# Performance work log

Measured on AMD Instinct MI355X. Metric: run time of the kernel, lower is better.

Reference implementation:

```python
import jax, jax.numpy as jnp
import numpy as np


def _grad(x, axis):
    """torch.gradient with unit spacing: central diff interior, one-sided edges."""
    def sl(a, b):
        idx = [slice(None)] * x.ndim
        idx[axis] = slice(a, b)
        return x[tuple(idx)]
    left = sl(1, 2) - sl(0, 1)                 # (x[1]-x[0])
    mid = (sl(2, None) - sl(0, -2)) * 0.5      # (x[i+1]-x[i-1])/2
    right = sl(-1, None) - sl(-2, -1)          # (x[-1]-x[-2])
    return jnp.concatenate([left, mid, right], axis=axis)


def _mse0(e):
    return jnp.mean(e * e)  # MSE against zeros


def _phy_loss(V_all, P_all, F_all, Re):
    Vy = V_all[:, :, :, :, 0, :]
    Vx = V_all[:, :, :, :, 1, :]
    Vz = V_all[:, :, :, :, 2, :]
    Fy = F_all[:, :, :, :, 0, :]
    Fx = F_all[:, :, :, :, 1, :]
    Fz = F_all[:, :, :, :, 2, :]
    # first derivatives (dims: 1=y, 2=x, 3=z, 4=t)
    dVydt, dVydy, dVydx, dVydz = _grad(Vy, 4), _grad(Vy, 1), _grad(Vy, 2), _grad(Vy, 3)
    dVxdt, dVxdy, dVxdx, dVxdz = _grad(Vx, 4), _grad(Vx, 1), _grad(Vx, 2), _grad(Vx, 3)
    dVzdt, dVzdy, dVzdx, dVzdz = _grad(Vz, 4), _grad(Vz, 1), _grad(Vz, 2), _grad(Vz, 3)
    dPdx, dPdy, dPdz = _grad(P_all, 2), _grad(P_all, 1), _grad(P_all, 3)
    # second derivatives
    lapVx = _grad(dVxdx, 2) + _grad(dVxdy, 1) + _grad(dVxdz, 3)
    lapVy = _grad(dVydx, 2) + _grad(dVydy, 1) + _grad(dVydz, 3)
    lapVz = _grad(dVzdx, 2) + _grad(dVzdy, 1) + _grad(dVzdz, 3)
    e1 = dVydt + (Vx * dVydx + Vy * dVydy + Vz * dVydz + dPdy) - Re * lapVy + Fy
    e2 = dVxdt + (Vx * dVxdx + Vy * dVxdy + Vz * dVxdz + dPdx) - Re * lapVx + Fx
    e3 = dVzdt + (Vx * dVzdx + Vy * dVzdy + Vz * dVzdz + dPdz) - Re * lapVz + Fz
    e4 = dVxdx + dVydy + dVzdz
    return _mse0(e1) + _mse0(e2) + _mse0(e3) + _mse0(e4)


def _time_loss(C_all, Y_data, X_last):
    Y_last = jnp.concatenate([X_last, Y_data[:, :, :, :, :-1]], axis=4)
    t1 = jnp.mean((Y_last - Y_data) ** 2)
    t2 = jnp.mean((C_all - Y_data) ** 2)
    return jnp.where(jax.lax.stop_gradient(t1) < jax.lax.stop_gradient(t2), t2 - t1, 0.0)


def setup_inputs() -> dict:
    key = jax.random.key(0)
    ks = jax.random.split(key, 9)
    B, S, T = 2, 48, 16
    f = jnp.float32
    return {
        "C_all": jax.random.normal(ks[0], (B, S, S, S, T), f),
        "V_all": jax.random.normal(ks[1], (B, S, S, S, 3, T), f),
        "P_all": jax.random.normal(ks[2], (B, S, S, S, T), f),
        "X_all": jax.random.normal(ks[3], (B, S, S, S, T), f),
        "X1_all": jax.random.normal(ks[4], (B, S, S, S, T), f),
        "F_all": jax.random.normal(ks[5], (B, S, S, S, 3, T), f),
        "Re": jnp.ones((1,), f),
        "X_last": jax.random.normal(ks[6], (B, S, S, S, 1), f),
        "Y_data": jax.random.normal(ks[7], (B, S, S, S, T), f),
        "maskd0": jnp.ones((1,), f),
        "maskd1": jnp.ones((1,), f),
        "maskd2": jnp.ones((1,), f),
    }


def reference(C_all, V_all, P_all, X_all, X1_all, F_all, Re, X_last, Y_data, maskd0, maskd1, maskd2):
    main1 = jnp.mean((X1_all - Y_data) ** 2)
    main2 = jnp.mean((X_all - Y_data) ** 2)
    phy = _phy_loss(V_all, P_all, F_all, Re)
    tl = _time_loss(C_all, Y_data, X_last)
    return (main1, main2, phy, tl)
```

## Files before the change

kernel.cpp:

```cpp
#include <hip/hip_runtime.h>

#define S 48
#define T 16
#define NTOT (2 * S * S * S * T)

__device__ __forceinline__ float d1(const float* __restrict__ fc, int i, int N, int stride) {
    int dl = (i > 0) ? -stride : 0;
    int dr = (i < N - 1) ? stride : 0;
    float w = (i > 0 && i < N - 1) ? 0.5f : 1.0f;
    return (fc[dr] - fc[dl]) * w;
}

__device__ __forceinline__ float d2c(const float* __restrict__ fc, int i, int N, int stride) {
    int j0, j1, j2;
    float c0, c1, c2;
    if (i == 0)          { j0 = 0;  j1 = 1;  j2 = 2; c0 = 0.5f;  c1 = -1.0f;  c2 = 0.5f;  }
    else if (i == 1)     { j0 = -1; j1 = 0;  j2 = 2; c0 = 0.5f;  c1 = -0.75f; c2 = 0.25f; }
    else if (i == N - 1) { j0 = -2; j1 = -1; j2 = 0; c0 = 0.5f;  c1 = -1.0f;  c2 = 0.5f;  }
    else if (i == N - 2) { j0 = -2; j1 = 0;  j2 = 1; c0 = 0.25f; c1 = -0.75f; c2 = 0.5f;  }
    else                 { j0 = -2; j1 = 0;  j2 = 2; c0 = 0.25f; c1 = -0.5f;  c2 = 0.25f; }
    return c0 * fc[j0 * stride] + c1 * fc[j1 * stride] + c2 * fc[j2 * stride];
}

__global__ __launch_bounds__(256) void fused_loss(
    const float* __restrict__ Cmat, const float* __restrict__ V,
    const float* __restrict__ P, const float* __restrict__ Xa,
    const float* __restrict__ X1a, const float* __restrict__ F,
    const float* __restrict__ Rep, const float* __restrict__ Xlast,
    const float* __restrict__ Y, float* __restrict__ ws)
{
    const float re = Rep[0];
    float am1 = 0.f, am2 = 0.f, aphy = 0.f, at1 = 0.f, at2 = 0.f;

    const int gstride = gridDim.x * blockDim.x;
    for (int n = blockIdx.x * blockDim.x + threadIdx.x; n < NTOT; n += gstride) {
        const int t  = n & (T - 1);
        const int sp = n >> 4;
        const int z  = sp % S;
        const int r1 = sp / S;
        const int x  = r1 % S;
        const int y  = (r1 / S) % S;

        const float yv  = Y[n];
        const float dm1 = X1a[n] - yv;
        const float dm2 = Xa[n] - yv;
        am1 += dm1 * dm1;
        am2 += dm2 * dm2;
        const float yprev = (t == 0) ? Xlast[sp] : Y[n - 1];
        const float dt1 = yprev - yv;
        const float dt2 = Cmat[n] - yv;
        at1 += dt1 * dt1;
        at2 += dt2 * dt2;

        const float* Pc = P + n;
        const float dPdz = d1(Pc, z, S, 16);
        const float dPdx = d1(Pc, x, S, 768);
        const float dPdy = d1(Pc, y, S, 36864);

        const int vbase = sp * 48 + t;
        const float* Vy_c = V + vbase;
        const float* Vx_c = V + vbase + 16;
        const float* Vz_c = V + vbase + 32;

        const float vy = *Vy_c, vx = *Vx_c, vz = *Vz_c;

        const float dVydt = d1(Vy_c, t, T, 1);
        const float dVydz = d1(Vy_c, z, S, 48);
        const float dVydx = d1(Vy_c, x, S, 2304);
        const float dVydy = d1(Vy_c, y, S, 110592);
        const float lapVy = d2c(Vy_c, z, S, 48) + d2c(Vy_c, x, S, 2304) + d2c(Vy_c, y, S, 110592);

        const float dVxdt = d1(Vx_c, t, T, 1);
        const float dVxdz = d1(Vx_c, z, S, 48);
        const float dVxdx = d1(Vx_c, x, S, 2304);
        const float dVxdy = d1(Vx_c, y, S, 110592);
        const float lapVx = d2c(Vx_c, z, S, 48) + d2c(Vx_c, x, S, 2304) + d2c(Vx_c, y, S, 110592);

        const float dVzdt = d1(Vz_c, t, T, 1);
        const float dVzdz = d1(Vz_c, z, S, 48);
        const float dVzdx = d1(Vz_c, x, S, 2304);
        const float dVzdy = d1(Vz_c, y, S, 110592);
        const float lapVz = d2c(Vz_c, z, S, 48) + d2c(Vz_c, x, S, 2304) + d2c(Vz_c, y, S, 110592);

        const float fy = F[vbase], fx = F[vbase + 16], fz = F[vbase + 32];

        const float e1 = dVydt + (vx * dVydx + vy * dVydy + vz * dVydz + dPdy) - re * lapVy + fy;
        const float e2 = dVxdt + (vx * dVxdx + vy * dVxdy + vz * dVxdz + dPdx) - re * lapVx + fx;
        const float e3 = dVzdt + (vx * dVzdx + vy * dVzdy + vz * dVzdz + dPdz) - re * lapVz + fz;
        const float e4 = dVxdx + dVydy + dVzdz;

        aphy += e1 * e1 + e2 * e2 + e3 * e3 + e4 * e4;
    }

    #pragma unroll
    for (int off = 32; off > 0; off >>= 1) {
        am1  += __shfl_down(am1, off);
        am2  += __shfl_down(am2, off);
        aphy += __shfl_down(aphy, off);
        at1  += __shfl_down(at1, off);
        at2  += __shfl_down(at2, off);
    }
    __shared__ float sred[4][5];
    const int lane = threadIdx.x & 63;
    const int wv   = threadIdx.x >> 6;
    if (lane == 0) {
        sred[wv][0] = am1; sred[wv][1] = am2; sred[wv][2] = aphy;
        sred[wv][3] = at1; sred[wv][4] = at2;
    }
    __syncthreads();
    if (threadIdx.x == 0) {
        float s0 = 0.f, s1 = 0.f, s2 = 0.f, s3 = 0.f, s4 = 0.f;
        #pragma unroll
        for (int w = 0; w < 4; ++w) {
            s0 += sred[w][0]; s1 += sred[w][1]; s2 += sred[w][2];
            s3 += sred[w][3]; s4 += sred[w][4];
        }
        atomicAdd(&ws[0], s0);
        atomicAdd(&ws[1], s1);
        atomicAdd(&ws[2], s2);
        atomicAdd(&ws[3], s3);
        atomicAdd(&ws[4], s4);
    }
}

__global__ void finalize_kernel(const float* __restrict__ ws, float* __restrict__ out) {
    const float invN = 1.0f / (float)NTOT;
    const float m1  = ws[0] * invN;
    const float m2  = ws[1] * invN;
    const float phy = ws[2] * invN;
    const float t1  = ws[3] * invN;
    const float t2  = ws[4] * invN;
    out[0] = m1;
    out[1] = m2;
    out[2] = phy;
    out[3] = (t1 < t2) ? (t2 - t1) : 0.0f;
}

extern "C" void kernel_launch(void* const* d_in, const int* in_sizes, int n_in,
                              void* d_out, int out_size, void* d_ws, size_t ws_size,
                              hipStream_t stream) {
    const float* Cmat  = (const float*)d_in[0];
    const float* V     = (const float*)d_in[1];
    const float* P     = (const float*)d_in[2];
    const float* Xa    = (const float*)d_in[3];
    const float* X1a   = (const float*)d_in[4];
    const float* F     = (const float*)d_in[5];
    const float* Rep   = (const float*)d_in[6];
    const float* Xlast = (const float*)d_in[7];
    const float* Y     = (const float*)d_in[8];

    float* ws  = (float*)d_ws;
    float* out = (float*)d_out;

    hipMemsetAsync(ws, 0, 5 * sizeof(float), stream);
    fused_loss<<<1024, 256, 0, stream>>>(Cmat, V, P, Xa, X1a, F, Rep, Xlast, Y, ws);
    finalize_kernel<<<1, 1, 0, stream>>>(ws, out);
}
```

Baseline: 272.3 us.

## Vectorize loss kernel to four time steps per thread with float4 loads

Each thread now handles four consecutive time samples, loading every input and stencil neighbour as a 16-byte vector instead of scalar loads. The time derivative is computed from the loaded vector plus two edge scalars. The grid-stride loop is replaced by one element group per thread, so the grid grows to cover the whole problem with many more blocks and atomics. The aim is fewer load instructions and better memory coalescing, at the cost of higher register pressure.

```diff
diff --git a/kernel.cpp b/kernel.cpp
--- a/kernel.cpp
+++ b/kernel.cpp
@@ -3,15 +3,23 @@
 #define S 48
 #define T 16
 #define NTOT (2 * S * S * S * T)
+#define NV4  (NTOT / 4)
+#define NBLK (NV4 / 256)
 
-__device__ __forceinline__ float d1(const float* __restrict__ fc, int i, int N, int stride) {
-    int dl = (i > 0) ? -stride : 0;
-    int dr = (i < N - 1) ? stride : 0;
-    float w = (i > 0 && i < N - 1) ? 0.5f : 1.0f;
-    return (fc[dr] - fc[dl]) * w;
+using f4 = __attribute__((ext_vector_type(4))) float;
+
+__device__ __forceinline__ f4 ld4(const float* __restrict__ p) {
+    return *reinterpret_cast<const f4*>(p);
 }
 
-__device__ __forceinline__ float d2c(const float* __restrict__ fc, int i, int N, int stride) {
+__device__ __forceinline__ f4 d1v(const float* __restrict__ fc, int i, int N, int stride) {
+    const int dl = (i > 0) ? -stride : 0;
+    const int dr = (i < N - 1) ? stride : 0;
+    const float w = (i > 0 && i < N - 1) ? 0.5f : 1.0f;
+    return (ld4(fc + dr) - ld4(fc + dl)) * w;
+}
+
+__device__ __forceinline__ f4 d2cv(const float* __restrict__ fc, int i, int N, int stride) {
     int j0, j1, j2;
     float c0, c1, c2;
     if (i == 0)          { j0 = 0;  j1 = 1;  j2 = 2; c0 = 0.5f;  c1 = -1.0f;  c2 = 0.5f;  }
@@ -19,7 +27,18 @@
     else if (i == N - 1) { j0 = -2; j1 = -1; j2 = 0; c0 = 0.5f;  c1 = -1.0f;  c2 = 0.5f;  }
     else if (i == N - 2) { j0 = -2; j1 = 0;  j2 = 1; c0 = 0.25f; c1 = -0.75f; c2 = 0.5f;  }
     else                 { j0 = -2; j1 = 0;  j2 = 2; c0 = 0.25f; c1 = -0.5f;  c2 = 0.25f; }
-    return c0 * fc[j0 * stride] + c1 * fc[j1 * stride] + c2 * fc[j2 * stride];
+    return c0 * ld4(fc + j0 * stride) + c1 * ld4(fc + j1 * stride) + c2 * ld4(fc + j2 * stride);
+}
+
+__device__ __forceinline__ f4 dtv(const float* __restrict__ fc, f4 c, int t0) {
+    const float left  = (t0 > 0)     ? fc[-1] : 0.f;
+    const float right = (t0 < T - 4) ? fc[4]  : 0.f;
+    f4 r;
+    r[0] = (t0 == 0)     ? (c[1] - c[0]) : 0.5f * (c[1] - left);
+    r[1] = 0.5f * (c[2] - c[0]);
+    r[2] = 0.5f * (c[3] - c[1]);
+    r[3] = (t0 == T - 4) ? (c[3] - c[2]) : 0.5f * (right - c[2]);
+    return r;
 }
 
 __global__ __launch_bounds__(256) void fused_loss(
@@ -30,82 +49,97 @@
     const float* __restrict__ Y, float* __restrict__ ws)
 {
     const float re = Rep[0];
-    float am1 = 0.f, am2 = 0.f, aphy = 0.f, at1 = 0.f, at2 = 0.f;
 
-    const int gstride = gridDim.x * blockDim.x;
-    for (int n = blockIdx.x * blockDim.x + threadIdx.x; n < NTOT; n += gstride) {
-        const int t  = n & (T - 1);
-        const int sp = n >> 4;
-        const int z  = sp % S;
-        const int r1 = sp / S;
-        const int x  = r1 % S;
-        const int y  = (r1 / S) % S;
+    const int idx = blockIdx.x * 256 + threadIdx.x;
+    const int t0  = (idx & 3) * 4;
+    const int sp  = idx >> 2;
+    const int z   = sp % S;
+    const int r1  = sp / S;
+    const int x   = r1 % S;
+    const int y   = (r1 / S) % S;
 
-        const float yv  = Y[n];
-        const float dm1 = X1a[n] - yv;
-        const float dm2 = Xa[n] - yv;
-        am1 += dm1 * dm1;
-        am2 += dm2 * dm2;
-        const float yprev = (t == 0) ? Xlast[sp] : Y[n - 1];
-        const float dt1 = yprev - yv;
-        const float dt2 = Cmat[n] - yv;
-        at1 += dt1 * dt1;
-        at2 += dt2 * dt2;
+    const int n4    = sp * T + t0;
+    const int vbase = sp * 48 + t0;
 
-        const float* Pc = P + n;
-        const float dPdz = d1(Pc, z, S, 16);
-        const float dPdx = d1(Pc, x, S, 768);
-        const float dPdy = d1(Pc, y, S, 36864);
+    const f4 yv  = ld4(Y + n4);
+    const f4 dm1 = ld4(X1a + n4) - yv;
+    const f4 dm2 = ld4(Xa + n4) - yv;
+    f4 yp;
+    yp[0] = (t0 == 0) ? Xlast[sp] : Y[n4 - 1];
+    yp[1] = yv[0]; yp[2] = yv[1]; yp[3] = yv[2];
+    const f4 dt1 = yp - yv;
+    const f4 dt2 = ld4(Cmat + n4) - yv;
 
-        const int vbase = sp * 48 + t;
-        const float* Vy_c = V + vbase;
-        const float* Vx_c = V + vbase + 16;
-        const float* Vz_c = V + vbase + 32;
+    f4 am1 = dm1 * dm1;
+    f4 am2 = dm2 * dm2;
+    f4 at1 = dt1 * dt1;
+    f4 at2 = dt2 * dt2;
 
-        const float vy = *Vy_c, vx = *Vx_c, vz = *Vz_c;
+    const float* Pc = P + n4;
+    const f4 dPdz = d1v(Pc, z, S, 16);
+    const f4 dPdx = d1v(Pc, x, S, 768);
+    const f4 dPdy = d1v(Pc, y, S, 36864);
 
-        const float dVydt = d1(Vy_c, t, T, 1);
-        const float dVydz = d1(Vy_c, z, S, 48);
-        const float dVydx = d1(Vy_c, x, S, 2304);
-        const float dVydy = d1(Vy_c, y, S, 110592);
-        const float lapVy = d2c(Vy_c, z, S, 48) + d2c(Vy_c, x, S, 2304) + d2c(Vy_c, y, S, 110592);
+    const float* Vyc = V + vbase;
+    const float* Vxc = V + vbase + 16;
+    const float* Vzc = V + vbase + 32;
+    const f4 cy = ld4(Vyc), cx = ld4(Vxc), cz = ld4(Vzc);
 
-        const float dVxdt = d1(Vx_c, t, T, 1);
-        const float dVxdz = d1(Vx_c, z, S, 48);
-        const float dVxdx = d1(Vx_c, x, S, 2304);
-        const float dVxdy = d1(Vx_c, y, S, 110592);
-        const float lapVx = d2c(Vx_c, z, S, 48) + d2c(Vx_c, x, S, 2304) + d2c(Vx_c, y, S, 110592);
+    f4 aphy;
+    f4 div;
 
-        const float dVzdt = d1(Vz_c, t, T, 1);
-        const float dVzdz = d1(Vz_c, z, S, 48);
-        const float dVzdx = d1(Vz_c, x, S, 2304);
-        const float dVzdy = d1(Vz_c, y, S, 110592);
-        const float lapVz = d2c(Vz_c, z, S, 48) + d2c(Vz_c, x, S, 2304) + d2c(Vz_c, y, S, 110592);
+    {
+        const f4 ddt = dtv(Vyc, cy, t0);
+        const f4 ddz = d1v(Vyc, z, S, 48);
+        const f4 ddx = d1v(Vyc, x, S, 2304);
+        const f4 ddy = d1v(Vyc, y, S, 110592);
+        const f4 lap = d2cv(Vyc, z, S, 48) + d2cv(Vyc, x, S, 2304) + d2cv(Vyc, y, S, 110592);
+        const f4 e1  = ddt + (cx * ddx + cy * ddy + cz * ddz + dPdy) - re * lap + ld4(F + vbase);
+        aphy = e1 * e1;
+        div  = ddy;
+    }
+    {
+        const f4 ddt = dtv(Vxc, cx, t0);
+        const f4 ddz = d1v(Vxc, z, S, 48);
+        const f4 ddx = d1v(Vxc, x, S, 2304);
+        const f4 ddy = d1v(Vxc, y, S, 110592);
+        const f4 lap = d2cv(Vxc, z, S, 48) + d2cv(Vxc, x, S, 2304) + d2cv(Vxc, y, S, 110592);
+        const f4 e2  = ddt + (cx * ddx + cy * ddy + cz * ddz + dPdx) - re * lap + ld4(F + vbase + 16);
+        aphy += e2 * e2;
+        div  += ddx;
+    }
+    {
+        const f4 ddt = dtv(Vzc, cz, t0);
+        const f4 ddz = d1v(Vzc, z, S, 48);
+        const f4 ddx = d1v(Vzc, x, S, 2304);
+        const f4 ddy = d1v(Vzc, y, S, 110592);
+        const f4 lap = d2cv(Vzc, z, S, 48) + d2cv(Vzc, x, S, 2304) + d2cv(Vzc, y, S, 110592);
+        const f4 e3  = ddt + (cx * ddx + cy * ddy + cz * ddz + dPdz) - re * lap + ld4(F + vbase + 32);
+        aphy += e3 * e3;
+        div  += ddz;
+        aphy += div * div;
+    }
 
-        const float fy = F[vbase], fx = F[vbase + 16], fz = F[vbase + 32];
-
-        const float e1 = dVydt + (vx * dVydx + vy * dVydy + vz * dVydz + dPdy) - re * lapVy + fy;
-        const float e2 = dVxdt + (vx * dVxdx + vy * dVxdy + vz * dVxdz + dPdx) - re * lapVx + fx;
-        const float e3 = dVzdt + (vx * dVzdx + vy * dVzdy + vz * dVzdz + dPdz) - re * lapVz + fz;
-        const float e4 = dVxdx + dVydy + dVzdz;
-
-        aphy += e1 * e1 + e2 * e2 + e3 * e3 + e4 * e4;
-    }
+    float sm1 = am1[0] + am1[1] + am1[2] + am1[3];
+    float sm2 = am2[0] + am2[1] + am2[2] + am2[3];
+    float sph = aphy[0] + aphy[1] + aphy[2] + aphy[3];
+    float st1 = at1[0] + at1[1] + at1[2] + at1[3];
+    float st2 = at2[0] + at2[1] + at2[2] + at2[3];
 
     #pragma unroll
     for (int off = 32; off > 0; off >>= 1) {
-        am1  += __shfl_down(am1, off);
-        am2  += __shfl_down(am2, off);
-        aphy += __shfl_down(aphy, off);
-        at1  += __shfl_down(at1, off);
-        at2  += __shfl_down(at2, off);
+        sm1 += __shfl_down(sm1, off);
+        sm2 += __shfl_down(sm2, off);
+        sph += __shfl_down(sph, off);
+        st1 += __shfl_down(st1, off);
+        st2 += __shfl_down(st2, off);
     }
     __shared__ float sred[4][5];
     const int lane = threadIdx.x & 63;
     const int wv   = threadIdx.x >> 6;
     if (lane == 0) {
-        sred[wv][0] = am1; sred[wv][1] = am2; sred[wv][2] = aphy;
-        sred[wv][3] = at1; sred[wv][4] = at2;
+        sred[wv][0] = sm1; sred[wv][1] = sm2; sred[wv][2] = sph;
+        sred[wv][3] = st1; sred[wv][4] = st2;
     }
     __syncthreads();
     if (threadIdx.x == 0) {
@@ -153,6 +187,6 @@
     float* out = (float*)d_out;
 
     hipMemsetAsync(ws, 0, 5 * sizeof(float), stream);
-    fused_loss<<<1024, 256, 0, stream>>>(Cmat, V, P, Xa, X1a, F, Rep, Xlast, Y, ws);
+    fused_loss<<<NBLK, 256, 0, stream>>>(Cmat, V, P, Xa, X1a, F, Rep, Xlast, Y, ws);
     finalize_kernel<<<1, 1, 0, stream>>>(ws, out);
 }
```

After: 375.4 us. 1.38x slower.
